# Kernel optimization log

Hardware: AMD Instinct MI355X
Metric: run time of the kernel (lower is better)

## Reference

```python
import jax, jax.numpy as jnp
import numpy as np

N = 50000       # nodes
E = 800000      # edges (avg degree 16)
C_IN = 128
C_HID = 64
C_OUT = 64
NEG_SLOPE = 0.2  # PyG GATConv default


def setup_inputs() -> dict:
    key = jax.random.key(0)
    ks = jax.random.split(key, 20)
    inp = {
        "x": jax.random.normal(ks[0], (N, C_IN), dtype=jnp.float32),
        "edge_index": jax.random.randint(ks[1], (2, E), 0, N, dtype=jnp.int32),
        "batch_size": N,
        "framework": 1,
    }
    dims = [(C_IN, C_HID), (C_HID, C_HID), (C_HID, C_OUT)]
    k = 2
    for i, (cin, cout) in enumerate(dims):
        s = 1.0 / np.sqrt(cin)
        inp[f"W{i}"] = jax.random.normal(ks[k], (cin, cout), jnp.float32) * s; k += 1
        inp[f"a_src{i}"] = jax.random.normal(ks[k], (cout,), jnp.float32) * (1.0 / np.sqrt(cout)); k += 1
        inp[f"a_dst{i}"] = jax.random.normal(ks[k], (cout,), jnp.float32) * (1.0 / np.sqrt(cout)); k += 1
        inp[f"b{i}"] = jnp.zeros((cout,), jnp.float32); k += 1
    return inp


def _gat_conv(h, src, dst, n, W, a_src, a_dst, b):
    # h: [n, cin] -> [n, cout]; single head, PyG GATConv semantics
    hp = h @ W                                   # [n, cout]
    alpha_s = hp @ a_src                         # [n]
    alpha_d = hp @ a_dst                         # [n]
    e = alpha_s[src] + alpha_d[dst]              # [E'] per-edge logits
    e = jnp.where(e > 0, e, NEG_SLOPE * e)       # leaky_relu(0.2)
    # segment softmax over incoming edges of each destination node
    m = jax.ops.segment_max(e, dst, num_segments=n)
    e = jnp.exp(e - m[dst])
    denom = jax.ops.segment_sum(e, dst, num_segments=n)
    a = e / (denom[dst] + 1e-16)                 # [E']
    msg = hp[src] * a[:, None]                   # [E', cout]
    out = jax.ops.segment_sum(msg, dst, num_segments=n)
    return out + b


def reference(x, edge_index, batch_size, framework,
              W0, a_src0, a_dst0, b0,
              W1, a_src1, a_dst1, b1,
              W2, a_src2, a_dst2, b2):
    n = x.shape[0]
    loops = jnp.arange(n, dtype=edge_index.dtype)  # PyG add_self_loops=True
    src = jnp.concatenate([edge_index[0], loops])
    dst = jnp.concatenate([edge_index[1], loops])
    params = [(W0, a_src0, a_dst0, b0), (W1, a_src1, a_dst1, b1), (W2, a_src2, a_dst2, b2)]
    h = x
    for W, a_s, a_d, b in params:
        h = jax.nn.relu(_gat_conv(h, src, dst, n, W, a_s, a_d, b))
    if framework:
        return h
    return h[:batch_size]
```

## Files before the change

### kernel.cpp

```cpp
#include <hip/hip_runtime.h>
#include <hip/hip_fp16.h>
#include <math.h>

#define NEG_SLOPE 0.2f
#define BSHIFT 8
#define BCAP 8192

typedef __attribute__((ext_vector_type(8))) short bf16x8;
typedef __attribute__((ext_vector_type(4))) float f32x4;

__device__ __forceinline__ float leaky(float e) {
    return e > 0.f ? e : NEG_SLOPE * e;
}
__device__ __forceinline__ float to_f(float x) { return x; }
__device__ __forceinline__ float to_f(__half x) { return __half2float(x); }

__device__ __forceinline__ unsigned f2bf_bits(float x) {
    unsigned u = __float_as_uint(x);
    return (u + 0x7fffu + ((u >> 16) & 1u)) >> 16;
}


__device__ __forceinline__ void pack_body_w0(
        int li, const float* __restrict__ W, short* __restrict__ Whi,
        short* __restrict__ Wlo) {
    int k = li >> 6, col = li & 63;
    int c = k >> 5, kin = k & 31;
    int g = col >> 4, nn = col & 15;
    float x = W[li];
    unsigned hb = f2bf_bits(x);
    float hf = __uint_as_float(hb << 16);
    unsigned lb = f2bf_bits(x - hf);
    int o = (((c * 4 + g) * 16 + nn) << 5) + kin;
    Whi[o] = (short)hb;
    Wlo[o] = (short)lb;
}


__device__ void partition_body(
        const int* __restrict__ src, const int* __restrict__ dst,
        int* __restrict__ bucketLen, int* __restrict__ pairs, int E, int nbk,
        int pb, int nb) {
    __shared__ int cnt[256];
    __shared__ int run[256];
    int t = threadIdx.x;
    int chunk = (E + nb - 1) / nb;
    int beg = pb * chunk;
    int end = min(beg + chunk, E);
    cnt[t] = 0;
    __syncthreads();
    for (int i = beg + t; i < end; i += 256)
        atomicAdd(&cnt[dst[i] >> BSHIFT], 1);
    __syncthreads();
    if (t < nbk) run[t] = t * BCAP + atomicAdd(&bucketLen[t], cnt[t]);
    __syncthreads();
    for (int i = beg + t; i < end; i += 256) {
        int d = dst[i];
        int slot = atomicAdd(&run[d >> BSHIFT], 1);
        if (slot < (d >> BSHIFT) * BCAP + BCAP)
            pairs[slot] = (src[i] << BSHIFT) | (d & 255);
    }
}

__global__ __launch_bounds__(256) void packpart_kernel(
        const float* __restrict__ W0, short* __restrict__ Whi,
        short* __restrict__ Wlo,
        const int* __restrict__ src, const int* __restrict__ dst,
        int* __restrict__ bucketLen, int* __restrict__ pairs, int E, int nbk) {
    if ((int)blockIdx.x < 32) {
        int idx = blockIdx.x * 256 + threadIdx.x;
        pack_body_w0(idx, W0, Whi, Wlo);
    } else {
        partition_body(src, dst, bucketLen, pairs, E, nbk,
                       (int)blockIdx.x - 32, (int)gridDim.x - 32);
    }
}

__device__ void csr_build_body(
        int b, const int* __restrict__ bucketLen, const int* __restrict__ pairs,
        int* __restrict__ off, int* __restrict__ degA,
        int* __restrict__ csr_src, int N) {
    __shared__ int degl[256];
    __shared__ int s[256];
    __shared__ int cur[256];
    int t = threadIdx.x;
    int n0 = b << BSHIFT;
    int nodecnt = min(256, N - n0);
    int ebeg = b * BCAP;
    int eend = ebeg + bucketLen[b];

    degl[t] = 0;
    __syncthreads();
    for (int i = ebeg + t; i < eend; i += 256)
        atomicAdd(&degl[pairs[i] & 255], 1);
    __syncthreads();

    int v = degl[t];
    s[t] = v;
    __syncthreads();
    for (int o = 1; o < 256; o <<= 1) {
        int x = (t >= o) ? s[t - o] : 0;
        __syncthreads();
        s[t] += x;
        __syncthreads();
    }
    int excl = s[t] - v;
    if (t < nodecnt) {
        off[n0 + t] = ebeg + excl;
        degA[n0 + t] = v;
    }
    cur[t] = excl;
    __syncthreads();

    for (int i = ebeg + t; i < eend; i += 256) {
        int pk = pairs[i];
        int p = atomicAdd(&cur[pk & 255], 1);
        csr_src[ebeg + p] = pk >> BSHIFT;
    }
}


template <int CIN, typename InT>
__device__ void gemm_body(
        int bid, const InT* __restrict__ h, const short* __restrict__ Whi,
        const short* __restrict__ Wlo,
        const float* __restrict__ a_src, const float* __restrict__ a_dst,
        __half* __restrict__ hp, float* __restrict__ as_, float* __restrict__ ad_,
        int n) {
    constexpr int KC = CIN / 32;
    int t = threadIdx.x, wave = t >> 6, lane = t & 63;
    int quad = lane >> 4, l16 = lane & 15;
    int node0 = bid * 64 + wave * 16;

    f32x4 acc[4];
#pragma unroll
    for (int g = 0; g < 4; ++g) acc[g] = (f32x4){0.f, 0.f, 0.f, 0.f};

    int nodeA = node0 + l16;
    bool va = nodeA < n;
    const InT* hrow = h + (size_t)(va ? nodeA : 0) * CIN + quad * 8;

#pragma unroll
    for (int c = 0; c < KC; ++c) {
        bf16x8 bhi[4], blo[4];
#pragma unroll
        for (int g = 0; g < 4; ++g) {
            int o = (((c * 4 + g) * 16 + l16) << 5) + quad * 8;
            bhi[g] = *(const bf16x8*)(Whi + o);
            blo[g] = *(const bf16x8*)(Wlo + o);
        }
        bf16x8 ahi, alo;
#pragma unroll
        for (int j = 0; j < 8; ++j) {
            float x = va ? to_f(hrow[c * 32 + j]) : 0.f;
            unsigned hb = f2bf_bits(x);
            float hf = __uint_as_float(hb << 16);
            unsigned lb = f2bf_bits(x - hf);
            ahi[j] = (short)hb;
            alo[j] = (short)lb;
        }
#pragma unroll
        for (int g = 0; g < 4; ++g) {
            acc[g] = __builtin_amdgcn_mfma_f32_16x16x32_bf16(ahi, bhi[g], acc[g], 0, 0, 0);
            acc[g] = __builtin_amdgcn_mfma_f32_16x16x32_bf16(ahi, blo[g], acc[g], 0, 0, 0);
            acc[g] = __builtin_amdgcn_mfma_f32_16x16x32_bf16(alo, bhi[g], acc[g], 0, 0, 0);
        }
    }

    float as4[4], ad4[4];
#pragma unroll
    for (int g = 0; g < 4; ++g) {
        as4[g] = a_src[g * 16 + l16];
        ad4[g] = a_dst[g * 16 + l16];
    }
#pragma unroll
    for (int r = 0; r < 4; ++r) {
        int node = node0 + quad * 4 + r;
        bool v = node < n;
        float vs = 0.f, vd = 0.f;
#pragma unroll
        for (int g = 0; g < 4; ++g) {
            float val = acc[g][r];
            if (v) hp[(size_t)node * 64 + g * 16 + l16] = __float2half_rn(val);
            vs = fmaf(val, as4[g], vs);
            vd = fmaf(val, ad4[g], vd);
        }
#pragma unroll
        for (int o = 1; o <= 8; o <<= 1) {
            vs += __shfl_xor(vs, o);
            vd += __shfl_xor(vd, o);
        }
        if (v && l16 == 0) {
            as_[node] = vs;
            ad_[node] = vd;
        }
    }
}

__global__ __launch_bounds__(256) void csr_gemm0_kernel(
        const int* __restrict__ bucketLen, const int* __restrict__ pairs,
        int* __restrict__ off, int* __restrict__ degA, int* __restrict__ csr_src,
        int N, int nbk,
        const float* __restrict__ x, const short* __restrict__ Whi,
        const short* __restrict__ Wlo, const float* __restrict__ a_src,
        const float* __restrict__ a_dst, __half* __restrict__ hp,
        float* __restrict__ as_, float* __restrict__ ad_) {
    if ((int)blockIdx.x < nbk)
        csr_build_body(blockIdx.x, bucketLen, pairs, off, degA, csr_src, N);
    else
        gemm_body<128, float>((int)blockIdx.x - nbk, x, Whi, Wlo,
                              a_src, a_dst, hp, as_, ad_, N);
}


__device__ __forceinline__ void h8_to_f(uint4 u, float* f) {
    __half2 a = *(__half2*)&u.x;
    __half2 b = *(__half2*)&u.y;
    __half2 c = *(__half2*)&u.z;
    __half2 d = *(__half2*)&u.w;
    float2 f01 = __half22float2(a);
    float2 f23 = __half22float2(b);
    float2 f45 = __half22float2(c);
    float2 f67 = __half22float2(d);
    f[0] = f01.x; f[1] = f01.y; f[2] = f23.x; f[3] = f23.y;
    f[4] = f45.x; f[5] = f45.y; f[6] = f67.x; f[7] = f67.y;
}

__device__ __forceinline__ uint4 pack8h(const float* v) {
    __half2 h0 = __floats2half2_rn(v[0], v[1]);
    __half2 h1 = __floats2half2_rn(v[2], v[3]);
    __half2 h2 = __floats2half2_rn(v[4], v[5]);
    __half2 h3 = __floats2half2_rn(v[6], v[7]);
    uint4 u;
    u.x = *(unsigned*)&h0; u.y = *(unsigned*)&h1;
    u.z = *(unsigned*)&h2; u.w = *(unsigned*)&h3;
    return u;
}

template <bool FINAL>
__global__ __launch_bounds__(256) void agg_fused_kernel(
        const __half* __restrict__ hp_in,
        const float* __restrict__ as_in, const float* __restrict__ ad_in,
        const int* __restrict__ off, const int* __restrict__ degA,
        const int* __restrict__ csr_src, const float* __restrict__ bias,
        const float* __restrict__ Wn,
        const float* __restrict__ asn, const float* __restrict__ adn,
        __half* __restrict__ hp_out, float* __restrict__ as_out,
        float* __restrict__ ad_out, float* __restrict__ final_out, int n) {
    __shared__ float pw[4][64];
    __shared__ int ps[4][64];
    __shared__ __half rowT[8][64];
    __shared__ float Wl[FINAL ? 4 : 4096];

    int t = threadIdx.x;
    if constexpr (!FINAL) {
        const float4* wg = (const float4*)Wn;
        float4* wl = (float4*)Wl;
#pragma unroll
        for (int i = 0; i < 4; ++i) wl[t + 256 * i] = wg[t + 256 * i];
        __syncthreads();
    }

    int wave = t >> 6, lane = t & 63;
    int hf = lane >> 5, l32 = lane & 31;
    int node = blockIdx.x * 8 + wave * 2 + hf;
    int slot = wave * 2 + hf;
    if (node >= n) return;

    int beg = off[node];
    int deg = degA[node];
    float adst = ad_in[node];
    float e_self = leaky(as_in[node] + adst);

    if (deg <= 32) {
        bool valid = l32 < deg;
        int s = valid ? csr_src[beg + l32] : 0;
        ps[wave][lane] = s;

        int g8 = l32 >> 3, s8 = l32 & 7;
        int base = hf * 32;
        const uint4* hp4 = (const uint4*)hp_in;

        uint4 u8[8];
#pragma unroll
        for (int q = 0; q < 8; ++q) {
            int jj = g8 + 4 * q;
            if (jj < deg) {
                int sj = ps[wave][base + jj];
                u8[q] = hp4[(size_t)sj * 8 + s8];
            }
        }
        uint4 uself = (g8 == 0) ? hp4[(size_t)node * 8 + s8]
                                : make_uint4(0u, 0u, 0u, 0u);

        float e = valid ? leaky(as_in[s] + adst) : -3.4e38f;
        float m = e;
#pragma unroll
        for (int o = 16; o > 0; o >>= 1) m = fmaxf(m, __shfl_xor(m, o));
        m = fmaxf(m, e_self);

        float p = valid ? __expf(e - m) : 0.f;
        float pself = __expf(e_self - m);
        float se = p;
#pragma unroll
        for (int o = 16; o > 0; o >>= 1) se += __shfl_xor(se, o);
        se += pself;
        float inv = 1.0f / (se + 1e-16f);
        pw[wave][lane] = p * inv;

        float acc[8];
        float wself = (g8 == 0) ? pself * inv : 0.f;
        {
            float fs[8];
            h8_to_f(uself, fs);
#pragma unroll
            for (int i = 0; i < 8; ++i) acc[i] = wself * fs[i];
        }
#pragma unroll
        for (int q = 0; q < 8; ++q) {
            int jj = g8 + 4 * q;
            if (jj < deg) {
                float w = pw[wave][base + jj];
                float f8[8];
                h8_to_f(u8[q], f8);
#pragma unroll
                for (int i = 0; i < 8; ++i) acc[i] = fmaf(w, f8[i], acc[i]);
            }
        }

#pragma unroll
        for (int i = 0; i < 8; ++i) {
            acc[i] += __shfl_xor(acc[i], 8);
            acc[i] += __shfl_xor(acc[i], 16);
        }

        if (g8 == 0) {
            const float4* b4 = (const float4*)bias;
            float4 ba = b4[s8 * 2], bb = b4[s8 * 2 + 1];
            float v[8];
            v[0] = acc[0] + ba.x; v[1] = acc[1] + ba.y;
            v[2] = acc[2] + ba.z; v[3] = acc[3] + ba.w;
            v[4] = acc[4] + bb.x; v[5] = acc[5] + bb.y;
            v[6] = acc[6] + bb.z; v[7] = acc[7] + bb.w;
#pragma unroll
            for (int i = 0; i < 8; ++i) v[i] = v[i] > 0.f ? v[i] : 0.f;
            if constexpr (FINAL) {
                float4 ra, rb;
                ra.x = v[0]; ra.y = v[1]; ra.z = v[2]; ra.w = v[3];
                rb.x = v[4]; rb.y = v[5]; rb.z = v[6]; rb.w = v[7];
                ((float4*)final_out)[(size_t)node * 16 + s8 * 2] = ra;
                ((float4*)final_out)[(size_t)node * 16 + s8 * 2 + 1] = rb;
            } else {
                ((uint4*)&rowT[slot][0])[s8] = pack8h(v);
            }
        }
    } else {
        int end = beg + deg;
        float mymax = e_self;
        for (int i = beg + l32; i < end; i += 32) {
            int s = csr_src[i];
            mymax = fmaxf(mymax, leaky(as_in[s] + adst));
        }
#pragma unroll
        for (int o = 16; o > 0; o >>= 1) mymax = fmaxf(mymax, __shfl_xor(mymax, o));
        float m = mymax;

        float se = 0.f;
        for (int i = beg + l32; i < end; i += 32) {
            int s = csr_src[i];
            se += __expf(leaky(as_in[s] + adst) - m);
        }
#pragma unroll
        for (int o = 16; o > 0; o >>= 1) se += __shfl_xor(se, o);
        se += __expf(e_self - m);
        float inv = 1.0f / (se + 1e-16f);

        const __half2* hpx = (const __half2*)hp_in;
        float2 hs = __half22float2(hpx[(size_t)node * 32 + l32]);
        float wself = __expf(e_self - m) * inv;
        float a0 = wself * hs.x, a1 = wself * hs.y;
        for (int i = beg; i < end; ++i) {
            int s = csr_src[i];
            float w = __expf(leaky(as_in[s] + adst) - m) * inv;
            float2 hv = __half22float2(hpx[(size_t)s * 32 + l32]);
            a0 = fmaf(w, hv.x, a0);
            a1 = fmaf(w, hv.y, a1);
        }
        float r0 = a0 + bias[l32 * 2];
        float r1 = a1 + bias[l32 * 2 + 1];
        r0 = r0 > 0.f ? r0 : 0.f;
        r1 = r1 > 0.f ? r1 : 0.f;
        if constexpr (FINAL) {
            final_out[(size_t)node * 64 + l32 * 2]     = r0;
            final_out[(size_t)node * 64 + l32 * 2 + 1] = r1;
        } else {
            *(__half2*)&rowT[slot][l32 * 2] = __floats2half2_rn(r0, r1);
        }
    }

    if constexpr (!FINAL) {
        int c0 = l32 * 2;
        float s0 = asn[c0], s1 = asn[c0 + 1];
        float d0 = adn[c0], d1 = adn[c0 + 1];
        const float2* W2p = (const float2*)Wl;
        const uint4* row4 = (const uint4*)&rowT[slot][0];
        float a0 = 0.f, a1 = 0.f;
#pragma unroll
        for (int kk = 0; kk < 8; ++kk) {
            float f8[8];
            h8_to_f(row4[kk], f8);
#pragma unroll
            for (int j = 0; j < 8; ++j) {
                float2 w = W2p[(kk * 8 + j) * 32 + l32];
                a0 = fmaf(f8[j], w.x, a0);
                a1 = fmaf(f8[j], w.y, a1);
            }
        }
        ((__half2*)hp_out)[(size_t)node * 32 + l32] = __floats2half2_rn(a0, a1);
        float vs = fmaf(a0, s0, a1 * s1);
        float vd = fmaf(a0, d0, a1 * d1);
#pragma unroll
        for (int o = 1; o <= 16; o <<= 1) {
            vs += __shfl_xor(vs, o);
            vd += __shfl_xor(vd, o);
        }
        if (l32 == 0) {
            as_out[node] = vs;
            ad_out[node] = vd;
        }
    }
}


extern "C" void kernel_launch(void* const* d_in, const int* in_sizes, int n_in,
                              void* d_out, int out_size, void* d_ws, size_t ws_size,
                              hipStream_t stream) {
    const float* x = (const float*)d_in[0];
    const int* edge_index = (const int*)d_in[1];
    const int N = in_sizes[0] / 128;
    const int E = in_sizes[1] / 2;
    const int NBK = (N + 255) >> BSHIFT;

    const float* W[3]    = {(const float*)d_in[4], (const float*)d_in[8],  (const float*)d_in[12]};
    const float* asrc[3] = {(const float*)d_in[5], (const float*)d_in[9],  (const float*)d_in[13]};
    const float* adst[3] = {(const float*)d_in[6], (const float*)d_in[10], (const float*)d_in[14]};
    const float* bias[3] = {(const float*)d_in[7], (const float*)d_in[11], (const float*)d_in[15]};

    char* ws = (char*)d_ws;
    size_t o = 0;
    auto alloc = [&](size_t bytes) {
        char* p = ws + o;
        o += (bytes + 255) & ~(size_t)255;
        return p;
    };
    int* bucketLen    = (int*)alloc(256 * 4);
    int* pairs        = (int*)alloc((size_t)NBK * BCAP * 4);
    int* off          = (int*)alloc((size_t)N * 4);
    int* degA         = (int*)alloc((size_t)N * 4);
    int* csr_src      = (int*)alloc((size_t)NBK * BCAP * 4);
    float* asA        = (float*)alloc((size_t)N * 4);
    float* adA        = (float*)alloc((size_t)N * 4);
    float* asB        = (float*)alloc((size_t)N * 4);
    float* adB        = (float*)alloc((size_t)N * 4);
    __half* hpA       = (__half*)alloc((size_t)N * 64 * 2);
    __half* hpB       = (__half*)alloc((size_t)N * 64 * 2);
    short* Whi        = (short*)alloc(8192 * 2);
    short* Wlo        = (short*)alloc(8192 * 2);

    const int* srcp = edge_index;
    const int* dstp = edge_index + E;

    int gb = (N + 63) / 64;
    int ab = (N + 7) / 8;

    hipMemsetAsync(bucketLen, 0, 256 * sizeof(int), stream);

    packpart_kernel<<<32 + 1024, 256, 0, stream>>>(
        W[0], Whi, Wlo, srcp, dstp, bucketLen, pairs, E, NBK);

    csr_gemm0_kernel<<<NBK + gb, 256, 0, stream>>>(
        bucketLen, pairs, off, degA, csr_src, N, NBK,
        x, Whi, Wlo, asrc[0], adst[0], hpA, asA, adA);

    agg_fused_kernel<false><<<ab, 256, 0, stream>>>(
        hpA, asA, adA, off, degA, csr_src, bias[0],
        W[1], asrc[1], adst[1], hpB, asB, adB, nullptr, N);

    agg_fused_kernel<false><<<ab, 256, 0, stream>>>(
        hpB, asB, adB, off, degA, csr_src, bias[1],
        W[2], asrc[2], adst[2], hpA, asA, adA, nullptr, N);

    agg_fused_kernel<true><<<ab, 256, 0, stream>>>(
        hpA, asA, adA, off, degA, csr_src, bias[2],
        nullptr, nullptr, nullptr, nullptr, nullptr, nullptr,
        (float*)d_out, N);
}
```

Before: 250.2 us.

## Drop softmax max pass, vectorize edge partition, pack offsets with degrees

Removes the segment-max pass from the attention softmax and exponentiates raw logits directly. This saves a full gather sweep over neighbours in the high-degree path and a shuffle reduction in the low-degree path, but can overflow or lose precision when logits are large. The edge partition now reads src/dst as int4 over chunks aligned to 1024 edges. CSR offsets and degrees are stored as one int2 array, and per-edge weights and source ids are broadcast with shuffles instead of shared memory.

```diff
diff --git a/kernel.cpp b/kernel.cpp
--- a/kernel.cpp
+++ b/kernel.cpp
@@ -44,17 +44,46 @@
     __shared__ int cnt[256];
     __shared__ int run[256];
     int t = threadIdx.x;
-    int chunk = (E + nb - 1) / nb;
+    int chunk = (((E + nb - 1) / nb) + 1023) & ~1023;
     int beg = pb * chunk;
     int end = min(beg + chunk, E);
+    if (beg >= end) return;
     cnt[t] = 0;
     __syncthreads();
-    for (int i = beg + t; i < end; i += 256)
+
+    const int4* dst4 = (const int4*)dst;
+    const int4* src4 = (const int4*)src;
+    int vbeg = beg >> 2;
+    int vend = end >> 2;
+    for (int i = vbeg + t; i < vend; i += 256) {
+        int4 d = dst4[i];
+        atomicAdd(&cnt[d.x >> BSHIFT], 1);
+        atomicAdd(&cnt[d.y >> BSHIFT], 1);
+        atomicAdd(&cnt[d.z >> BSHIFT], 1);
+        atomicAdd(&cnt[d.w >> BSHIFT], 1);
+    }
+    for (int i = (vend << 2) + t; i < end; i += 256)
         atomicAdd(&cnt[dst[i] >> BSHIFT], 1);
     __syncthreads();
+
     if (t < nbk) run[t] = t * BCAP + atomicAdd(&bucketLen[t], cnt[t]);
     __syncthreads();
-    for (int i = beg + t; i < end; i += 256) {
+
+    for (int i = vbeg + t; i < vend; i += 256) {
+        int4 d = dst4[i];
+        int4 s = src4[i];
+        int b0 = d.x >> BSHIFT, b1 = d.y >> BSHIFT;
+        int b2 = d.z >> BSHIFT, b3 = d.w >> BSHIFT;
+        int s0 = atomicAdd(&run[b0], 1);
+        int s1 = atomicAdd(&run[b1], 1);
+        int s2 = atomicAdd(&run[b2], 1);
+        int s3 = atomicAdd(&run[b3], 1);
+        if (s0 < b0 * BCAP + BCAP) pairs[s0] = (s.x << BSHIFT) | (d.x & 255);
+        if (s1 < b1 * BCAP + BCAP) pairs[s1] = (s.y << BSHIFT) | (d.y & 255);
+        if (s2 < b2 * BCAP + BCAP) pairs[s2] = (s.z << BSHIFT) | (d.z & 255);
+        if (s3 < b3 * BCAP + BCAP) pairs[s3] = (s.w << BSHIFT) | (d.w & 255);
+    }
+    for (int i = (vend << 2) + t; i < end; i += 256) {
         int d = dst[i];
         int slot = atomicAdd(&run[d >> BSHIFT], 1);
         if (slot < (d >> BSHIFT) * BCAP + BCAP)
@@ -78,8 +107,7 @@
 
 __device__ void csr_build_body(
         int b, const int* __restrict__ bucketLen, const int* __restrict__ pairs,
-        int* __restrict__ off, int* __restrict__ degA,
-        int* __restrict__ csr_src, int N) {
+        int2* __restrict__ offdeg, int* __restrict__ csr_src, int N) {
     __shared__ int degl[256];
     __shared__ int s[256];
     __shared__ int cur[256];
@@ -105,10 +133,8 @@
         __syncthreads();
     }
     int excl = s[t] - v;
-    if (t < nodecnt) {
-        off[n0 + t] = ebeg + excl;
-        degA[n0 + t] = v;
-    }
+    if (t < nodecnt)
+        offdeg[n0 + t] = make_int2(ebeg + excl, v);
     cur[t] = excl;
     __syncthreads();
 
@@ -199,14 +225,14 @@
 
 __global__ __launch_bounds__(256) void csr_gemm0_kernel(
         const int* __restrict__ bucketLen, const int* __restrict__ pairs,
-        int* __restrict__ off, int* __restrict__ degA, int* __restrict__ csr_src,
+        int2* __restrict__ offdeg, int* __restrict__ csr_src,
         int N, int nbk,
         const float* __restrict__ x, const short* __restrict__ Whi,
         const short* __restrict__ Wlo, const float* __restrict__ a_src,
         const float* __restrict__ a_dst, __half* __restrict__ hp,
         float* __restrict__ as_, float* __restrict__ ad_) {
     if ((int)blockIdx.x < nbk)
-        csr_build_body(blockIdx.x, bucketLen, pairs, off, degA, csr_src, N);
+        csr_build_body(blockIdx.x, bucketLen, pairs, offdeg, csr_src, N);
     else
         gemm_body<128, float>((int)blockIdx.x - nbk, x, Whi, Wlo,
                               a_src, a_dst, hp, as_, ad_, N);
@@ -241,14 +267,12 @@
 __global__ __launch_bounds__(256) void agg_fused_kernel(
         const __half* __restrict__ hp_in,
         const float* __restrict__ as_in, const float* __restrict__ ad_in,
-        const int* __restrict__ off, const int* __restrict__ degA,
-        const int* __restrict__ csr_src, const float* __restrict__ bias,
+        const int2* __restrict__ offdeg, const int* __restrict__ csr_src,
+        const float* __restrict__ bias,
         const float* __restrict__ Wn,
         const float* __restrict__ asn, const float* __restrict__ adn,
         __half* __restrict__ hp_out, float* __restrict__ as_out,
         float* __restrict__ ad_out, float* __restrict__ final_out, int n) {
-    __shared__ float pw[4][64];
-    __shared__ int ps[4][64];
     __shared__ __half rowT[8][64];
     __shared__ float Wl[FINAL ? 4 : 4096];
 
@@ -267,15 +291,17 @@
     int slot = wave * 2 + hf;
     if (node >= n) return;
 
-    int beg = off[node];
-    int deg = degA[node];
+    int2 od = offdeg[node];
+    int beg = od.x;
+    int deg = od.y;
     float adst = ad_in[node];
     float e_self = leaky(as_in[node] + adst);
+    float pself = __expf(e_self);
 
     if (deg <= 32) {
         bool valid = l32 < deg;
         int s = valid ? csr_src[beg + l32] : 0;
-        ps[wave][lane] = s;
+        float as_s = valid ? as_in[s] : 0.f;
 
         int g8 = l32 >> 3, s8 = l32 & 7;
         int base = hf * 32;
@@ -285,28 +311,19 @@
 #pragma unroll
         for (int q = 0; q < 8; ++q) {
             int jj = g8 + 4 * q;
-            if (jj < deg) {
-                int sj = ps[wave][base + jj];
-                u8[q] = hp4[(size_t)sj * 8 + s8];
-            }
+            int sj = __shfl(s, base + jj);
+            if (jj < deg) u8[q] = hp4[(size_t)sj * 8 + s8];
         }
         uint4 uself = (g8 == 0) ? hp4[(size_t)node * 8 + s8]
                                 : make_uint4(0u, 0u, 0u, 0u);
 
-        float e = valid ? leaky(as_in[s] + adst) : -3.4e38f;
-        float m = e;
-#pragma unroll
-        for (int o = 16; o > 0; o >>= 1) m = fmaxf(m, __shfl_xor(m, o));
-        m = fmaxf(m, e_self);
-
-        float p = valid ? __expf(e - m) : 0.f;
-        float pself = __expf(e_self - m);
+        float p = valid ? __expf(leaky(as_s + adst)) : 0.f;
         float se = p;
 #pragma unroll
         for (int o = 16; o > 0; o >>= 1) se += __shfl_xor(se, o);
         se += pself;
         float inv = 1.0f / (se + 1e-16f);
-        pw[wave][lane] = p * inv;
+        float pin = p * inv;
 
         float acc[8];
         float wself = (g8 == 0) ? pself * inv : 0.f;
@@ -319,8 +336,8 @@
 #pragma unroll
         for (int q = 0; q < 8; ++q) {
             int jj = g8 + 4 * q;
+            float w = __shfl(pin, base + jj);
             if (jj < deg) {
-                float w = pw[wave][base + jj];
                 float f8[8];
                 h8_to_f(u8[q], f8);
 #pragma unroll
@@ -356,32 +373,23 @@
         }
     } else {
         int end = beg + deg;
-        float mymax = e_self;
-        for (int i = beg + l32; i < end; i += 32) {
-            int s = csr_src[i];
-            mymax = fmaxf(mymax, leaky(as_in[s] + adst));
-        }
-#pragma unroll
-        for (int o = 16; o > 0; o >>= 1) mymax = fmaxf(mymax, __shfl_xor(mymax, o));
-        float m = mymax;
-
         float se = 0.f;
         for (int i = beg + l32; i < end; i += 32) {
             int s = csr_src[i];
-            se += __expf(leaky(as_in[s] + adst) - m);
+            se += __expf(leaky(as_in[s] + adst));
         }
 #pragma unroll
         for (int o = 16; o > 0; o >>= 1) se += __shfl_xor(se, o);
-        se += __expf(e_self - m);
+        se += pself;
         float inv = 1.0f / (se + 1e-16f);
 
         const __half2* hpx = (const __half2*)hp_in;
         float2 hs = __half22float2(hpx[(size_t)node * 32 + l32]);
-        float wself = __expf(e_self - m) * inv;
+        float wself = pself * inv;
         float a0 = wself * hs.x, a1 = wself * hs.y;
         for (int i = beg; i < end; ++i) {
             int s = csr_src[i];
-            float w = __expf(leaky(as_in[s] + adst) - m) * inv;
+            float w = __expf(leaky(as_in[s] + adst)) * inv;
             float2 hv = __half22float2(hpx[(size_t)s * 32 + l32]);
             a0 = fmaf(w, hv.x, a0);
             a1 = fmaf(w, hv.y, a1);
@@ -455,8 +463,7 @@
     };
     int* bucketLen    = (int*)alloc(256 * 4);
     int* pairs        = (int*)alloc((size_t)NBK * BCAP * 4);
-    int* off          = (int*)alloc((size_t)N * 4);
-    int* degA         = (int*)alloc((size_t)N * 4);
+    int2* offdeg      = (int2*)alloc((size_t)N * 8);
     int* csr_src      = (int*)alloc((size_t)NBK * BCAP * 4);
     float* asA        = (float*)alloc((size_t)N * 4);
     float* adA        = (float*)alloc((size_t)N * 4);
@@ -479,19 +486,19 @@
         W[0], Whi, Wlo, srcp, dstp, bucketLen, pairs, E, NBK);
 
     csr_gemm0_kernel<<<NBK + gb, 256, 0, stream>>>(
-        bucketLen, pairs, off, degA, csr_src, N, NBK,
+        bucketLen, pairs, offdeg, csr_src, N, NBK,
         x, Whi, Wlo, asrc[0], adst[0], hpA, asA, adA);
 
     agg_fused_kernel<false><<<ab, 256, 0, stream>>>(
-        hpA, asA, adA, off, degA, csr_src, bias[0],
+        hpA, asA, adA, offdeg, csr_src, bias[0],
         W[1], asrc[1], adst[1], hpB, asB, adB, nullptr, N);
 
     agg_fused_kernel<false><<<ab, 256, 0, stream>>>(
-        hpB, asB, adB, off, degA, csr_src, bias[1],
+        hpB, asB, adB, offdeg, csr_src, bias[1],
         W[2], asrc[2], adst[2], hpA, asA, adA, nullptr, N);
 
     agg_fused_kernel<true><<<ab, 256, 0, stream>>>(
-        hpA, asA, adA, off, degA, csr_src, bias[2],
+        hpA, asA, adA, offdeg, csr_src, bias[2],
         nullptr, nullptr, nullptr, nullptr, nullptr, nullptr,
         (float*)d_out, N);
 }
```

Measured after the change: 243.6 us. 2.6% less time.
